# Optimization experiments

Hardware: AMD Instinct MI355X
Metric: run time of the kernel (lower is better)

## Reference

```python
import jax, jax.numpy as jnp
import numpy as np

D_MODEL = 768
NUM_HEADS = 12
D_K = D_MODEL // NUM_HEADS
WINDOW = 16
SPARSITY = 0.8
NEG = -1e9


def _pos_encoding(seq_len, d_model, dtype):
    pos = jnp.arange(seq_len, dtype=jnp.float32)[:, None]
    div = jnp.exp(jnp.arange(0, d_model, 2, dtype=jnp.float32) * (-np.log(10000.0) / d_model))
    pe = jnp.zeros((seq_len, d_model), dtype=jnp.float32)
    pe = pe.at[:, 0::2].set(jnp.sin(pos * div))
    pe = pe.at[:, 1::2].set(jnp.cos(pos * div))
    return pe.astype(dtype)


def _layernorm(x, gamma, beta, eps=1e-5):
    mu = jnp.mean(x, axis=-1, keepdims=True)
    var = jnp.mean(jnp.square(x - mu), axis=-1, keepdims=True)
    return (x - mu) * jax.lax.rsqrt(var + eps) * gamma + beta


def _split_heads(x):  # [B,S,D] -> [B,H,S,dk]
    b, s, _ = x.shape
    return x.reshape(b, s, NUM_HEADS, D_K).transpose(0, 2, 1, 3)


def _attn(q, k, v, mask):  # mask broadcastable to [B,H,S,S], bool
    scores = jnp.einsum('bhqd,bhkd->bhqk', q, k) / jnp.sqrt(jnp.asarray(D_K, q.dtype))
    scores = jnp.where(mask, scores, jnp.asarray(NEG, q.dtype))
    w = jax.nn.softmax(scores, axis=-1)
    out = jnp.einsum('bhqk,bhkd->bhqd', w, v)
    b, h, s, d = out.shape
    return out.transpose(0, 2, 1, 3).reshape(b, s, h * d)


def setup_inputs() -> dict:
    key = jax.random.key(0)
    ks = jax.random.split(key, 16)
    d = D_MODEL
    sc = 1.0 / np.sqrt(d)
    inp = {
        'x': jax.random.normal(ks[0], (2, 2048, d), jnp.float32),
        'wgq': jax.random.normal(ks[1], (d, d), jnp.float32) * sc,
        'wgk': jax.random.normal(ks[2], (d, d), jnp.float32) * sc,
        'wgv': jax.random.normal(ks[3], (d, d), jnp.float32) * sc,
        'wlq': jax.random.normal(ks[4], (d, d), jnp.float32) * sc,
        'wlk': jax.random.normal(ks[5], (d, d), jnp.float32) * sc,
        'wlv': jax.random.normal(ks[6], (d, d), jnp.float32) * sc,
        'wtq': jax.random.normal(ks[7], (d, d), jnp.float32) * sc,
        'wtk': jax.random.normal(ks[8], (d, d), jnp.float32) * sc,
        'wtv': jax.random.normal(ks[9], (d, d), jnp.float32) * sc,
        'w_out': jax.random.normal(ks[10], (3 * d, d), jnp.float32) * (1.0 / np.sqrt(3 * d)),
        'b_out': jnp.zeros((d,), jnp.float32),
        'w_gate': jax.random.normal(ks[11], (d, 3), jnp.float32) * sc,
        'b_gate': jnp.zeros((3,), jnp.float32),
        'w_sparse': jax.random.normal(ks[12], (d, 1), jnp.float32) * sc,
        'b_sparse': jnp.zeros((1,), jnp.float32),
        'g_gamma': jnp.ones((d,), jnp.float32), 'g_beta': jnp.zeros((d,), jnp.float32),
        'l_gamma': jnp.ones((d,), jnp.float32), 'l_beta': jnp.zeros((d,), jnp.float32),
        't_gamma': jnp.ones((d,), jnp.float32), 't_beta': jnp.zeros((d,), jnp.float32),
    }
    return inp


def reference(x, wgq, wgk, wgv, wlq, wlk, wlv, wtq, wtk, wtv,
              w_out, b_out, w_gate, b_gate, w_sparse, b_sparse,
              g_gamma, g_beta, l_gamma, l_beta, t_gamma, t_beta):
    b, s, d = x.shape
    # positional encoding branch input (dropout is identity at eval)
    x_pos = x + _pos_encoding(s, d, x.dtype)[None]

    # focus gate over mean-pooled tokens -> [B,3]
    fw = jax.nn.softmax(x.mean(axis=1) @ w_gate + b_gate, axis=-1)
    gw, lw, tw = fw[:, 0, None, None], fw[:, 1, None, None], fw[:, 2, None, None]

    # sparse (global) mask: keep top-k important columns per batch
    importance = (x @ w_sparse + b_sparse)[..., 0]  # [B,S]
    k = max(1, int((1.0 - SPARSITY) * s))
    _, topk_idx = jax.lax.top_k(importance, k)
    sparse = jnp.zeros((b, s), bool).at[jnp.arange(b)[:, None], topk_idx].set(True)
    sparse_mask = sparse[:, None, None, :]  # [B,1,1,S]

    idx = jnp.arange(s)
    rel = idx[None, :] - idx[:, None]
    half = WINDOW // 2
    local_mask = ((rel >= -half) & (rel <= half))[None, None]  # [1,1,S,S]

    stride = max(1, s // 8)
    temporal_cols = (idx % stride) == 0
    temporal_mask = jnp.broadcast_to(temporal_cols[None, :], (s, s))[None, None]

    # global branch
    g = _attn(_split_heads(x @ wgq), _split_heads(x @ wgk), _split_heads(x @ wgv), sparse_mask)
    g = _layernorm(g, g_gamma, g_beta)
    # local branch
    l = _attn(_split_heads(x @ wlq), _split_heads(x @ wlk), _split_heads(x @ wlv), local_mask)
    l = _layernorm(l, l_gamma, l_beta)
    # temporal branch (uses pos-encoded input)
    t = _attn(_split_heads(x_pos @ wtq), _split_heads(x_pos @ wtk), _split_heads(x_pos @ wtv), temporal_mask)
    t = _layernorm(t, t_gamma, t_beta)

    combined = jnp.concatenate([g * gw, l * lw, t * tw], axis=-1)
    return combined @ w_out + b_out
```

## Files before the change

### kernel.cpp

```cpp
#include <hip/hip_runtime.h>
#include <cstdint>

constexpr int BB   = 2;
constexpr int SS   = 2048;
constexpr int DD   = 768;
constexpr int HH   = 12;
constexpr int NTOK = BB * SS;
constexpr int KSEL = 409;
constexpr int KPAD = 448;
constexpr int NKT  = 7;

typedef __bf16 bf16x8 __attribute__((ext_vector_type(8)));
typedef float  f32x4  __attribute__((ext_vector_type(4)));

__device__ __forceinline__ float b2f(unsigned short u) {
  return __uint_as_float(((unsigned)u) << 16);
}
__device__ __forceinline__ unsigned short f2b(float f) {
  unsigned u = __float_as_uint(f);
  u += 0x7fffu + ((u >> 16) & 1u);
  return (unsigned short)(u >> 16);
}
__device__ __forceinline__ unsigned long long shfl_xor_u64(unsigned long long v, int m) {
  unsigned lo = (unsigned)v, hi = (unsigned)(v >> 32);
  lo = __shfl_xor(lo, m, 64);
  hi = __shfl_xor(hi, m, 64);
  return ((unsigned long long)hi << 32) | lo;
}

__device__ __forceinline__ void gload_lds16(const void* gsrc, void* ldst) {
  __builtin_amdgcn_global_load_lds(
      (__attribute__((address_space(1))) void*)(gsrc),
      (__attribute__((address_space(3))) void*)(ldst), 16, 0, 0);
}

__global__ __launch_bounds__(256) void prep_imp(const float* __restrict__ x,
                                                const float* __restrict__ wsp,
                                                const float* __restrict__ bsp,
                                                unsigned short* __restrict__ xb,
                                                unsigned short* __restrict__ xpb,
                                                float* __restrict__ imp) {
  int srow = blockIdx.x;
  int tid = threadIdx.x;
  const float* xr0 = x + (long)srow * DD;
  const float* xr1 = x + (long)(SS + srow) * DD;
  float acc0 = 0.f, acc1 = 0.f;
#pragma unroll
  for (int k = 0; k < 3; ++k) {
    int c = tid + k * 256;
    int j2 = c & ~1;
    float freq = __expf((float)j2 * -0.011992630692677323f);
    float ang = (float)srow * freq;
    float pe = (c & 1) ? cosf(ang) : sinf(ang);
    float w = wsp[c];
    float x0 = xr0[c], x1 = xr1[c];
    xb[(long)srow * DD + c]        = f2b(x0);
    xb[(long)(SS + srow) * DD + c] = f2b(x1);
    xpb[(long)srow * DD + c]        = f2b(x0 + pe);
    xpb[(long)(SS + srow) * DD + c] = f2b(x1 + pe);
    acc0 += x0 * w;
    acc1 += x1 * w;
  }
#pragma unroll
  for (int m = 1; m < 64; m <<= 1) {
    acc0 += __shfl_xor(acc0, m, 64);
    acc1 += __shfl_xor(acc1, m, 64);
  }
  __shared__ float red[8];
  int wv = tid >> 6, lane = tid & 63;
  if (lane == 0) { red[wv] = acc0; red[4 + wv] = acc1; }
  __syncthreads();
  if (tid == 0) {
    imp[srow]      = red[0] + red[1] + red[2] + red[3] + bsp[0];
    imp[SS + srow] = red[4] + red[5] + red[6] + red[7] + bsp[0];
  }
}

__global__ void transpose_all(const float* w0, const float* w1, const float* w2,
                              const float* w3, const float* w4, const float* w5,
                              const float* w6, const float* w7, const float* w8,
                              const float* w9,
                              unsigned short* WTx4, unsigned short* WTkv,
                              unsigned short* WTqt, unsigned short* WTtkv,
                              unsigned short* WTo) {
  __shared__ float tile[32][33];
  int id = blockIdx.x;
  int z, bx, by;
  if (id < 5184) { z = id / 576; int rem = id % 576; by = rem / 24; bx = rem % 24; }
  else           { z = 9; int rem = id - 5184; by = rem / 24; bx = rem % 24; }
  const float* srcs[10] = {w0, w1, w2, w3, w4, w5, w6, w7, w8, w9};
  const float* src = srcs[z];
  unsigned short* dst;
  int R = DD;
  switch (z) {
    case 0: dst = WTx4;                       break;
    case 1: dst = WTkv;                       break;
    case 2: dst = WTkv + (long)DD * DD;       break;
    case 3: dst = WTx4 + (long)DD * DD;       break;
    case 4: dst = WTx4 + (long)2 * DD * DD;   break;
    case 5: dst = WTx4 + (long)3 * DD * DD;   break;
    case 6: dst = WTqt;                       break;
    case 7: dst = WTtkv;                      break;
    case 8: dst = WTtkv + (long)DD * DD;      break;
    default: dst = WTo; R = 2304;             break;
  }
  int r0 = by * 32;
  int c0 = bx * 32;
  int tx = threadIdx.x, ty = threadIdx.y;
  for (int i = ty; i < 32; i += 8) tile[i][tx] = src[(long)(r0 + i) * DD + c0 + tx];
  __syncthreads();
  for (int i = ty; i < 32; i += 8) dst[(long)(c0 + i) * R + r0 + tx] = f2b(tile[tx][i]);
}

__global__ __launch_bounds__(1024) void topk_kernel(const float* __restrict__ imp,
                                                    int* __restrict__ sel) {
  __shared__ unsigned long long keys[SS];
  int b = blockIdx.x, tid = threadIdx.x;
  for (int i = tid; i < SS; i += 1024) {
    float v = imp[b * SS + i];
    unsigned u = __float_as_uint(v);
    u = (u & 0x80000000u) ? ~u : (u | 0x80000000u);
    unsigned du = ~u;
    keys[i] = ((unsigned long long)du << 32) | (unsigned)i;
  }
  __syncthreads();
  for (int k = 2; k <= SS; k <<= 1) {
    for (int j = k >> 1; j >= 64; j >>= 1) {
      for (int i = tid; i < SS; i += 1024) {
        int p = i ^ j;
        if (p > i) {
          unsigned long long a = keys[i], bb = keys[p];
          bool up = ((i & k) == 0);
          if ((a > bb) == up) { keys[i] = bb; keys[p] = a; }
        }
      }
      __syncthreads();
    }
    unsigned long long k0 = keys[tid], k1 = keys[tid + 1024];
    bool up0 = ((tid & k) == 0);
    bool up1 = (((tid + 1024) & k) == 0);
    int j0 = (k >> 1) < 32 ? (k >> 1) : 32;
    for (int j = j0; j >= 1; j >>= 1) {
      bool low = ((tid & j) == 0);
      unsigned long long p0 = shfl_xor_u64(k0, j);
      k0 = ((low == up0) == (k0 < p0)) ? k0 : p0;
      unsigned long long p1 = shfl_xor_u64(k1, j);
      k1 = ((low == up1) == (k1 < p1)) ? k1 : p1;
    }
    keys[tid] = k0; keys[tid + 1024] = k1;
    __syncthreads();
  }
  for (int i = tid; i < KSEL; i += 1024) sel[b * KSEL + i] = (int)(keys[i] & 0xffffffffu);
}

__global__ __launch_bounds__(256) void gate1(const float* __restrict__ x,
                                             float* __restrict__ partial) {
  int b = blockIdx.y, chunk = blockIdx.x, tid = threadIdx.x;
  for (int c = tid; c < DD; c += 256) {
    const float* xp = x + ((long)(b * SS + chunk * 128)) * DD + c;
    float acc = 0.f;
    for (int s2 = 0; s2 < 128; ++s2) acc += xp[(long)s2 * DD];
    partial[(long)(b * 16 + chunk) * DD + c] = acc;
  }
}

__global__ __launch_bounds__(256) void gate2(const float* __restrict__ partial,
                                             const float* __restrict__ w_gate,
                                             const float* __restrict__ b_gate,
                                             float* __restrict__ fw) {
  int b = blockIdx.x, tid = threadIdx.x;
  __shared__ float meanbuf[DD];
  __shared__ float lg[3];
  for (int c = tid; c < DD; c += 256) {
    float acc = 0.f;
    for (int p = 0; p < 16; ++p) acc += partial[(long)(b * 16 + p) * DD + c];
    meanbuf[c] = acc * (1.0f / (float)SS);
  }
  __syncthreads();
  if (tid < 3) {
    float acc = b_gate[tid];
    for (int d = 0; d < DD; ++d) acc += meanbuf[d] * w_gate[d * 3 + tid];
    lg[tid] = acc;
  }
  __syncthreads();
  if (tid == 0) {
    float mx = fmaxf(lg[0], fmaxf(lg[1], lg[2]));
    float e0 = expf(lg[0] - mx), e1 = expf(lg[1] - mx), e2 = expf(lg[2] - mx);
    float inv = 1.f / (e0 + e1 + e2);
    fw[b * 3 + 0] = e0 * inv; fw[b * 3 + 1] = e1 * inv; fw[b * 3 + 2] = e2 * inv;
  }
}

__global__ __launch_bounds__(192) void gather_pre(const unsigned short* __restrict__ xb,
                                                  const unsigned short* __restrict__ xpb,
                                                  const int* __restrict__ sel,
                                                  unsigned short* __restrict__ A_sel,
                                                  unsigned short* __restrict__ A_t8) {
  int id = blockIdx.x;
  int tid = threadIdx.x;
  if (id < BB * KPAD) {
    int b = id / KPAD, j = id % KPAD;
    uint2* dst = (uint2*)(A_sel + (long)id * DD);
    if (j < KSEL) {
      const uint2* src = (const uint2*)(xb + (long)(b * SS + sel[b * KSEL + j]) * DD);
      dst[tid] = src[tid];
    } else {
      dst[tid] = uint2{0u, 0u};
    }
  } else {
    int r = id - BB * KPAD;
    uint2* dst = (uint2*)(A_t8 + (long)r * DD);
    if (r < 16) {
      int b = r >> 3, j = (r & 7) * 256;
      const uint2* src = (const uint2*)(xpb + (long)(b * SS + j) * DD);
      dst[tid] = src[tid];
    } else {
      dst[tid] = uint2{0u, 0u};
    }
  }
}

__global__ __launch_bounds__(256) void gemm_multi(
    const unsigned short* __restrict__ xb,    const unsigned short* __restrict__ WTx4,
    unsigned short* __restrict__ QKV4,
    const unsigned short* __restrict__ A_sel, const unsigned short* __restrict__ WTkv,
    unsigned short* __restrict__ KVg,
    const unsigned short* __restrict__ xpb,   const unsigned short* __restrict__ WTqt,
    unsigned short* __restrict__ Qt,
    const unsigned short* __restrict__ A_t8,  const unsigned short* __restrict__ WTtkv,
    unsigned short* __restrict__ K8, unsigned short* __restrict__ Vt8,
    unsigned short* __restrict__ Vt, unsigned short* __restrict__ Vtl) {
  __shared__ unsigned short smem[16512];
  unsigned short* AsB = smem;
  unsigned short* BsB = smem + 8192;
  constexpr int K = DD;
  const int tid = threadIdx.x;
  const int lane = tid & 63;
  const int wv = tid >> 6;
  const int wr = wv >> 1, wc = wv & 1;

  int lin = blockIdx.x;
  int swz = (lin & 7) * 132 + (lin >> 3);
  const unsigned short *A, *BT;
  unsigned short* C;
  int N, ntx, tile, mode;
  if (swz < 768)       { A = xb;    BT = WTx4;  C = QKV4; N = 3072; ntx = 24; tile = swz;
                         mode = ((tile % 24) >= 18) ? 1 : 0; }
  else if (swz < 852)  { A = A_sel; BT = WTkv;  C = KVg;  N = 1536; ntx = 12; tile = swz - 768;
                         mode = ((tile % 12) >= 6) ? 2 : 0; }
  else if (swz < 1044) { A = xpb;   BT = WTqt;  C = Qt;   N = 768;  ntx = 6;  tile = swz - 852;
                         mode = 0; }
  else                 { A = A_t8;  BT = WTtkv; C = nullptr; N = 1536; ntx = 12; tile = swz - 1044;
                         mode = ((tile % 12) >= 6) ? 4 : 3; }
  const long rowBase = (long)(tile / ntx) * 128;
  const long colBase = (long)(tile % ntx) * 128;
  const int vcol0 = (mode == 1) ? (int)colBase - 2304
                  : (mode == 2 || mode == 4) ? (int)colBase - 768 : 0;

  f32x4 acc[4][4];
#pragma unroll
  for (int i = 0; i < 4; ++i)
#pragma unroll
    for (int j = 0; j < 4; ++j)
#pragma unroll
      for (int r = 0; r < 4; ++r) acc[i][j][r] = 0.f;

  const int g0 = tid, g1 = tid + 256;
  const int r0 = g0 >> 2, k80 = (g0 & 3) ^ ((r0 >> 1) & 3);
  const int r1 = g1 >> 2, k81 = (g1 & 3) ^ ((r1 >> 1) & 3);
  const unsigned short* ga0 = A + (rowBase + r0) * (long)K + k80 * 8;
  const unsigned short* ga1 = A + (rowBase + r1) * (long)K + k81 * 8;
  const unsigned short* gb0 = BT + (colBase + r0) * (long)K + k80 * 8;
  const unsigned short* gb1 = BT + (colBase + r1) * (long)K + k81 * 8;

  const int k8 = lane >> 4;
  const int fr = lane & 15;
  int aoff[4], boff[4];
#pragma unroll
  for (int i = 0; i < 4; ++i) {
    int rowA = wr * 64 + i * 16 + fr;
    aoff[i] = (rowA * 4 + (k8 ^ ((rowA >> 1) & 3))) * 8;
    int rowB = wc * 64 + i * 16 + fr;
    boff[i] = (rowB * 4 + (k8 ^ ((rowB >> 1) & 3))) * 8;
  }

  auto stage = [&](int buf, int t) {
    int ko = t * 32;
    gload_lds16(ga0 + ko, &AsB[buf * 4096 + g0 * 8]);
    gload_lds16(ga1 + ko, &AsB[buf * 4096 + g1 * 8]);
    gload_lds16(gb0 + ko, &BsB[buf * 4096 + g0 * 8]);
    gload_lds16(gb1 + ko, &BsB[buf * 4096 + g1 * 8]);
  };

  constexpr int nk = K >> 5;
  stage(0, 0);
  __syncthreads();
  for (int t = 0; t < nk; ++t) {
    int cur = t & 1;
    if (t + 1 < nk) stage(cur ^ 1, t + 1);
    bf16x8 af[4], bfr[4];
#pragma unroll
    for (int i = 0; i < 4; ++i) af[i] = *(const bf16x8*)(&AsB[cur * 4096 + aoff[i]]);
#pragma unroll
    for (int i = 0; i < 4; ++i) bfr[i] = *(const bf16x8*)(&BsB[cur * 4096 + boff[i]]);
#pragma unroll
    for (int mi = 0; mi < 4; ++mi)
#pragma unroll
      for (int ni = 0; ni < 4; ++ni)
        acc[mi][ni] = __builtin_amdgcn_mfma_f32_16x16x32_bf16(af[mi], bfr[ni], acc[mi][ni], 0, 0, 0);
    __syncthreads();
  }

  const int orow0 = (lane >> 4) * 4;
  if (mode == 0) {
#pragma unroll
    for (int mi = 0; mi < 4; ++mi) {
      long gr = rowBase + wr * 64 + mi * 16 + orow0;
#pragma unroll
      for (int ni = 0; ni < 4; ++ni) {
        long gc = colBase + wc * 64 + ni * 16 + fr;
#pragma unroll
        for (int r = 0; r < 4; ++r)
          C[(gr + r) * (long)N + gc] = f2b(acc[mi][ni][r]);
      }
    }
  } else {
    unsigned short* Ct = smem;
#pragma unroll
    for (int mi = 0; mi < 4; ++mi) {
      int lr = wr * 64 + mi * 16 + orow0;
#pragma unroll
      for (int ni = 0; ni < 4; ++ni) {
        int lc = wc * 64 + ni * 16 + fr;
#pragma unroll
        for (int r = 0; r < 4; ++r)
          Ct[(lr + r) * 129 + lc] = f2b(acc[mi][ni][r]);
      }
    }
    __syncthreads();
    if (mode == 1) {
#pragma unroll
      for (int e = 0; e < 8; ++e) {
        int id = tid + e * 256;
        int c = id >> 4, sc = id & 15;
        int grow = (int)rowBase + sc * 8;
        int bb2 = grow >> 11, s = grow & (SS - 1);
        union { unsigned short s8[8]; uint4 v; } u;
#pragma unroll
        for (int k2 = 0; k2 < 8; ++k2) u.s8[k2] = Ct[(sc * 8 + k2) * 129 + c];
        *(uint4*)(Vtl + ((long)bb2 * DD + vcol0 + c) * SS + s) = u.v;
      }
    } else if (mode == 2) {
#pragma unroll
      for (int e = 0; e < 8; ++e) {
        int id = tid + e * 256;
        int c = id >> 4, sc = id & 15;
        int grow = (int)rowBase + sc * 8;
        int bb2 = grow / KPAD, j = grow % KPAD;
        union { unsigned short s8[8]; uint4 v; } u;
#pragma unroll
        for (int k2 = 0; k2 < 8; ++k2) u.s8[k2] = Ct[(sc * 8 + k2) * 129 + c];
        *(uint4*)(Vt + ((long)bb2 * DD + vcol0 + c) * KPAD + j) = u.v;
      }
    } else if (mode == 3) {
#pragma unroll
      for (int e = 0; e < 2; ++e) {
        int id = tid + e * 256;
        int row = id >> 4;
        int bb2 = row >> 4, jj = row & 15;
        int c8 = id & 15;
        int srcrow = (jj < 8) ? bb2 * 8 + jj : 16 + jj;
        union { unsigned short s8[8]; uint4 v; } u;
#pragma unroll
        for (int k2 = 0; k2 < 8; ++k2) u.s8[k2] = Ct[srcrow * 129 + c8 * 8 + k2];
        *(uint4*)(K8 + ((long)bb2 * 16 + jj) * DD + colBase + c8 * 8) = u.v;
      }
    } else {
#pragma unroll
      for (int e = 0; e < 4; ++e) {
        int id = tid + e * 256;
        int bb2 = id >> 9;
        int rem = id & 511;
        int c = rem >> 2, jc = rem & 3;
        union { unsigned short s8[8]; uint4 v; } u;
        if (jc == 0) {
#pragma unroll
          for (int k2 = 0; k2 < 8; ++k2) u.s8[k2] = Ct[(bb2 * 8 + k2) * 129 + c];
        } else {
#pragma unroll
          for (int k2 = 0; k2 < 8; ++k2) u.s8[k2] = 0;
        }
        *(uint4*)(Vt8 + ((long)bb2 * DD + vcol0 + c) * 32 + jc * 8) = u.v;
      }
    }
  }
}

__global__ __launch_bounds__(256) void gemm_final_sk(const unsigned short* __restrict__ A,
                                                     const unsigned short* __restrict__ BT,
                                                     float* __restrict__ Cpart) {
  __shared__ unsigned short As[2][128 * 32];
  __shared__ unsigned short Bs[2][128 * 32];
  constexpr int N = 768, K = 2304, CK = 768;
  const int tid = threadIdx.x;
  const int lane = tid & 63;
  const int wv = tid >> 6;
  const int wr = wv >> 1, wc = wv & 1;
  const int z = blockIdx.z;

  int lin = blockIdx.y * gridDim.x + blockIdx.x;
  int swz = (lin & 7) * 24 + (lin >> 3);
  const long rowBase = (long)(swz / 6) * 128;
  const long colBase = (long)(swz % 6) * 128;

  f32x4 acc[4][4];
#pragma unroll
  for (int i = 0; i < 4; ++i)
#pragma unroll
    for (int j = 0; j < 4; ++j)
#pragma unroll
      for (int r = 0; r < 4; ++r) acc[i][j][r] = 0.f;

  const int g0 = tid, g1 = tid + 256;
  const int r0 = g0 >> 2, k80 = (g0 & 3) ^ ((r0 >> 1) & 3);
  const int r1 = g1 >> 2, k81 = (g1 & 3) ^ ((r1 >> 1) & 3);
  const unsigned short* ga0 = A + (rowBase + r0) * (long)K + z * CK + k80 * 8;
  const unsigned short* ga1 = A + (rowBase + r1) * (long)K + z * CK + k81 * 8;
  const unsigned short* gb0 = BT + (colBase + r0) * (long)K + z * CK + k80 * 8;
  const unsigned short* gb1 = BT + (colBase + r1) * (long)K + z * CK + k81 * 8;

  const int k8 = lane >> 4;
  const int fr = lane & 15;
  int aoff[4], boff[4];
#pragma unroll
  for (int i = 0; i < 4; ++i) {
    int rowA = wr * 64 + i * 16 + fr;
    aoff[i] = (rowA * 4 + (k8 ^ ((rowA >> 1) & 3))) * 8;
    int rowB = wc * 64 + i * 16 + fr;
    boff[i] = (rowB * 4 + (k8 ^ ((rowB >> 1) & 3))) * 8;
  }

  auto stage = [&](int buf, int t) {
    int ko = t * 32;
    gload_lds16(ga0 + ko, &As[buf][g0 * 8]);
    gload_lds16(ga1 + ko, &As[buf][g1 * 8]);
    gload_lds16(gb0 + ko, &Bs[buf][g0 * 8]);
    gload_lds16(gb1 + ko, &Bs[buf][g1 * 8]);
  };

  constexpr int nk = CK >> 5;
  stage(0, 0);
  __syncthreads();
  for (int t = 0; t < nk; ++t) {
    int cur = t & 1;
    if (t + 1 < nk) stage(cur ^ 1, t + 1);
    bf16x8 af[4], bfr[4];
#pragma unroll
    for (int i = 0; i < 4; ++i) af[i] = *(const bf16x8*)(&As[cur][aoff[i]]);
#pragma unroll
    for (int i = 0; i < 4; ++i) bfr[i] = *(const bf16x8*)(&Bs[cur][boff[i]]);
#pragma unroll
    for (int mi = 0; mi < 4; ++mi)
#pragma unroll
      for (int ni = 0; ni < 4; ++ni)
        acc[mi][ni] = __builtin_amdgcn_mfma_f32_16x16x32_bf16(af[mi], bfr[ni], acc[mi][ni], 0, 0, 0);
    __syncthreads();
  }

  float* Cz = Cpart + (long)z * NTOK * DD;
  const int orow0 = (lane >> 4) * 4;
#pragma unroll
  for (int mi = 0; mi < 4; ++mi) {
    long gr = rowBase + wr * 64 + mi * 16 + orow0;
#pragma unroll
    for (int ni = 0; ni < 4; ++ni) {
      long gc = colBase + wc * 64 + ni * 16 + fr;
#pragma unroll
      for (int r = 0; r < 4; ++r)
        Cz[(gr + r) * (long)N + gc] = acc[mi][ni][r];
    }
  }
}

__global__ __launch_bounds__(256) void reduce_out(const float* __restrict__ P,
                                                  const float* __restrict__ bias,
                                                  float* __restrict__ out) {
  long i = (long)blockIdx.x * 256 + threadIdx.x;
  const f32x4* p0 = (const f32x4*)P;
  const f32x4* p1 = (const f32x4*)(P + (long)NTOK * DD);
  const f32x4* p2 = (const f32x4*)(P + 2L * NTOK * DD);
  f32x4 v = p0[i];
  v += p1[i];
  v += p2[i];
  int c4 = (int)(i % (DD / 4));
  v += *(const f32x4*)(bias + c4 * 4);
  ((f32x4*)out)[i] = v;
}

__device__ __forceinline__ void attn_flash_body(
    const unsigned short* __restrict__ QKV4,
    const unsigned short* __restrict__ KVg,
    const unsigned short* __restrict__ Vt,
    float* __restrict__ Outp,
    unsigned short* smem) {
  unsigned short* Kl = smem;
  unsigned short* Vl = smem + 8192;
  unsigned short* Pl = smem + 16384;
  int tid = threadIdx.x, w = tid >> 6, lane = tid & 63;
  int fr = lane & 15, g = lane >> 4;
  int b = blockIdx.y / HH, h = blockIdx.y % HH, hoff = h * 64;
  int qbase = blockIdx.x * 64 + w * 16;
  long qrow = (long)b * SS + qbase + fr;

  const unsigned short* qptr = QKV4 + qrow * 3072 + hoff + g * 8;
  bf16x8 bq0 = *(const bf16x8*)(qptr);
  bf16x8 bq1 = *(const bf16x8*)(qptr + 32);

  const int s0 = tid, s1 = tid + 256;
  const int r0 = s0 >> 3, c0 = (s0 & 7) ^ (r0 & 7);
  const int r1 = s1 >> 3, c1 = (s1 & 7) ^ (r1 & 7);
  const unsigned short* kg_b = KVg + (long)b * KPAD * 1536 + hoff;
  const unsigned short* vt_b = Vt + ((long)b * DD + hoff) * KPAD;

  auto stage = [&](int buf, int t0) {
    gload_lds16(kg_b + (long)(t0 * 64 + r0) * 1536 + c0 * 8, &Kl[buf * 4096 + s0 * 8]);
    gload_lds16(kg_b + (long)(t0 * 64 + r1) * 1536 + c1 * 8, &Kl[buf * 4096 + s1 * 8]);
    gload_lds16(vt_b + (long)r0 * KPAD + t0 * 64 + c0 * 8, &Vl[buf * 4096 + s0 * 8]);
    gload_lds16(vt_b + (long)r1 * KPAD + t0 * 64 + c1 * 8, &Vl[buf * 4096 + s1 * 8]);
  };

  f32x4 oacc[4];
#pragma unroll
  for (int mf = 0; mf < 4; ++mf)
#pragma unroll
    for (int r = 0; r < 4; ++r) oacc[mf][r] = 0.f;
  float m = -3.0e38f, l = 0.f;

  stage(0, 0);
  asm volatile("s_waitcnt vmcnt(0)" ::: "memory");
  __syncthreads();

  for (int t = 0; t < NKT; ++t) {
    int cur = t & 1;
    if (t + 1 < NKT) stage(cur ^ 1, t + 1);

    f32x4 st[4];
#pragma unroll
    for (int kt = 0; kt < 4; ++kt) {
      int row = kt * 16 + fr;
      bf16x8 a0 = *(const bf16x8*)(&Kl[cur * 4096 + (row * 8 + (g ^ (row & 7))) * 8]);
      bf16x8 a1 = *(const bf16x8*)(&Kl[cur * 4096 + (row * 8 + ((4 + g) ^ (row & 7))) * 8]);
      f32x4 z = {0.f, 0.f, 0.f, 0.f};
      z = __builtin_amdgcn_mfma_f32_16x16x32_bf16(a0, bq0, z, 0, 0, 0);
      st[kt] = __builtin_amdgcn_mfma_f32_16x16x32_bf16(a1, bq1, z, 0, 0, 0);
    }

    float tm = -3.0e38f;
#pragma unroll
    for (int kt = 0; kt < 4; ++kt)
#pragma unroll
      for (int r = 0; r < 4; ++r) {
        int key = t * 64 + kt * 16 + g * 4 + r;
        float s = (key < KSEL) ? st[kt][r] * 0.125f : -1.0e30f;
        st[kt][r] = s;
        tm = fmaxf(tm, s);
      }
    tm = fmaxf(tm, __shfl_xor(tm, 16, 64));
    tm = fmaxf(tm, __shfl_xor(tm, 32, 64));
    float newm = fmaxf(m, tm);
    float f = __expf(m - newm);
    float tsum = 0.f;
#pragma unroll
    for (int kt = 0; kt < 4; ++kt)
#pragma unroll
      for (int r = 0; r < 4; ++r) {
        float e = __expf(st[kt][r] - newm);
        st[kt][r] = e;
        tsum += e;
      }
    tsum += __shfl_xor(tsum, 16, 64);
    tsum += __shfl_xor(tsum, 32, 64);
    l = l * f + tsum;
    m = newm;
#pragma unroll
    for (int mf = 0; mf < 4; ++mf)
#pragma unroll
      for (int r = 0; r < 4; ++r) oacc[mf][r] *= f;

    unsigned short* pw = &Pl[w * 1088 + fr * 68 + g * 4];
#pragma unroll
    for (int kt = 0; kt < 4; ++kt) {
      uint2 pk;
      pk.x = (unsigned)f2b(st[kt][0]) | ((unsigned)f2b(st[kt][1]) << 16);
      pk.y = (unsigned)f2b(st[kt][2]) | ((unsigned)f2b(st[kt][3]) << 16);
      *(uint2*)(pw + kt * 16) = pk;
    }

    const unsigned short* prd = &Pl[w * 1088 + fr * 68];
#pragma unroll
    for (int ks2 = 0; ks2 < 2; ++ks2) {
      bf16x8 pf = *(const bf16x8*)(prd + ks2 * 32 + g * 8);
#pragma unroll
      for (int mf = 0; mf < 4; ++mf) {
        int vr = mf * 16 + fr;
        int vc = ks2 * 4 + g;
        bf16x8 vf = *(const bf16x8*)(&Vl[cur * 4096 + (vr * 8 + (vc ^ (vr & 7))) * 8]);
        oacc[mf] = __builtin_amdgcn_mfma_f32_16x16x32_bf16(vf, pf, oacc[mf], 0, 0, 0);
      }
    }

    asm volatile("s_waitcnt vmcnt(0)" ::: "memory");
    __syncthreads();
  }

  float inv = 1.f / l;
  float* orow = Outp + qrow * DD + hoff;
#pragma unroll
  for (int mf = 0; mf < 4; ++mf) {
    f32x4 ov;
#pragma unroll
    for (int r = 0; r < 4; ++r) ov[r] = oacc[mf][r] * inv;
    *(f32x4*)(orow + mf * 16 + g * 4) = ov;
  }
}

__device__ __forceinline__ void attn_win_body(
    const unsigned short* __restrict__ QKV,
    const unsigned short* __restrict__ K8,
    const unsigned short* __restrict__ Vt,
    float* __restrict__ Outp,
    int LD, int QO, long VSTR, bool local,
    unsigned short* smem) {
  int tid = threadIdx.x, w = tid >> 6, lane = tid & 63;
  int fr = lane & 15, g = lane >> 4;
  int b = blockIdx.y / HH, h = blockIdx.y % HH, hoff = h * 64;
  int qbase = blockIdx.x * 64 + w * 16;
  long qrow = (long)b * SS + qbase + fr;

  const unsigned short* qptr = QKV + qrow * LD + QO + hoff + g * 8;
  bf16x8 bq0 = *(const bf16x8*)(qptr);
  bf16x8 bq1 = *(const bf16x8*)(qptr + 32);

  int kstart = qbase - 8;
  if (kstart < 0) kstart = 0;
  if (kstart > SS - 32) kstart = SS - 32;

  f32x4 st[2];
  if (local) {
#pragma unroll
    for (int kt = 0; kt < 2; ++kt) {
      const unsigned short* kp =
          QKV + ((long)b * SS + kstart + kt * 16 + fr) * LD + 1536 + hoff + g * 8;
      bf16x8 a0 = *(const bf16x8*)(kp);
      bf16x8 a1 = *(const bf16x8*)(kp + 32);
      f32x4 z = {0.f, 0.f, 0.f, 0.f};
      z = __builtin_amdgcn_mfma_f32_16x16x32_bf16(a0, bq0, z, 0, 0, 0);
      st[kt] = __builtin_amdgcn_mfma_f32_16x16x32_bf16(a1, bq1, z, 0, 0, 0);
    }
  } else {
    const unsigned short* kp = K8 + ((long)b * 16 + fr) * DD + hoff + g * 8;
    bf16x8 a0 = *(const bf16x8*)(kp);
    bf16x8 a1 = *(const bf16x8*)(kp + 32);
    f32x4 z = {0.f, 0.f, 0.f, 0.f};
    z = __builtin_amdgcn_mfma_f32_16x16x32_bf16(a0, bq0, z, 0, 0, 0);
    st[0] = __builtin_amdgcn_mfma_f32_16x16x32_bf16(a1, bq1, z, 0, 0, 0);
    st[1] = f32x4{0.f, 0.f, 0.f, 0.f};
  }

  float m = -3.0e38f;
#pragma unroll
  for (int kt = 0; kt < 2; ++kt)
#pragma unroll
    for (int r = 0; r < 4; ++r) {
      int idx = kt * 16 + g * 4 + r;
      bool valid;
      if (local) {
        int rel = kstart + idx - qbase - fr;
        valid = (rel >= -8) && (rel <= 8);
      } else {
        valid = (idx < 8);
      }
      float s = valid ? st[kt][r] * 0.125f : -1.0e30f;
      st[kt][r] = s;
      m = fmaxf(m, s);
    }
  m = fmaxf(m, __shfl_xor(m, 16, 64));
  m = fmaxf(m, __shfl_xor(m, 32, 64));

  float lsum = 0.f;
#pragma unroll
  for (int kt = 0; kt < 2; ++kt)
#pragma unroll
    for (int r = 0; r < 4; ++r) {
      float e = __expf(st[kt][r] - m);
      st[kt][r] = e;
      lsum += e;
    }
  lsum += __shfl_xor(lsum, 16, 64);
  lsum += __shfl_xor(lsum, 32, 64);

  unsigned short* pl = smem + w * 640 + fr * 40 + g * 4;
#pragma unroll
  for (int kt = 0; kt < 2; ++kt) {
    uint2 pk;
    pk.x = (unsigned)f2b(st[kt][0]) | ((unsigned)f2b(st[kt][1]) << 16);
    pk.y = (unsigned)f2b(st[kt][2]) | ((unsigned)f2b(st[kt][3]) << 16);
    *(uint2*)(pl + kt * 16) = pk;
  }

  f32x4 oacc[4];
#pragma unroll
  for (int mf = 0; mf < 4; ++mf)
#pragma unroll
    for (int r = 0; r < 4; ++r) oacc[mf][r] = 0.f;

  const unsigned short* pr = smem + w * 640 + fr * 40 + g * 8;
  bf16x8 pf = *(const bf16x8*)(pr);
  long kb2 = local ? kstart : 0;
#pragma unroll
  for (int mf = 0; mf < 4; ++mf) {
    const unsigned short* vp =
        Vt + ((long)b * DD + hoff + mf * 16 + fr) * VSTR + kb2 + g * 8;
    bf16x8 vf = *(const bf16x8*)(vp);
    oacc[mf] = __builtin_amdgcn_mfma_f32_16x16x32_bf16(vf, pf, oacc[mf], 0, 0, 0);
  }

  float inv = 1.f / lsum;
  float* orow = Outp + qrow * DD + hoff;
#pragma unroll
  for (int mf = 0; mf < 4; ++mf) {
    f32x4 ov;
#pragma unroll
    for (int r = 0; r < 4; ++r) ov[r] = oacc[mf][r] * inv;
    *(f32x4*)(orow + mf * 16 + g * 4) = ov;
  }
}

__global__ __launch_bounds__(256) void attn_all(
    const unsigned short* __restrict__ QKV4,
    const unsigned short* __restrict__ KVg,
    const unsigned short* __restrict__ Vt,
    const unsigned short* __restrict__ Qt,
    const unsigned short* __restrict__ K8,
    const unsigned short* __restrict__ Vt8,
    const unsigned short* __restrict__ Vtl,
    float* __restrict__ gout, float* __restrict__ lout, float* __restrict__ tout) {
  __shared__ unsigned short smem[20736];
  int z = blockIdx.z;
  if (z == 0) {
    attn_flash_body(QKV4, KVg, Vt, gout, smem);
  } else if (z == 1) {
    attn_win_body(QKV4, nullptr, Vtl, lout, 3072, 768, SS, true, smem);
  } else {
    attn_win_body(Qt, K8, Vt8, tout, 768, 0, 32, false, smem);
  }
}

__global__ __launch_bounds__(256) void ln_gate_concat(
    const float* __restrict__ gsrc, const float* __restrict__ lsrc, const float* __restrict__ tsrc,
    const float* __restrict__ gg, const float* __restrict__ gb,
    const float* __restrict__ lgam, const float* __restrict__ lbet,
    const float* __restrict__ tg, const float* __restrict__ tb,
    const float* __restrict__ fw, unsigned short* __restrict__ comb) {
  int row = blockIdx.x;
  int b = row >> 11;
  int tid = threadIdx.x;
  __shared__ float red[8];
  const float* srcs[3] = {gsrc, lsrc, tsrc};
  const float* gams[3] = {gg, lgam, tg};
  const float* bets[3] = {gb, lbet, tb};
#pragma unroll
  for (int br = 0; br < 3; ++br) {
    const float* src = srcs[br] + (long)row * DD;
    float x0 = src[tid], x1 = src[tid + 256], x2 = src[tid + 512];
    float s = x0 + x1 + x2;
    float ss = x0 * x0 + x1 * x1 + x2 * x2;
#pragma unroll
    for (int msk = 1; msk < 64; msk <<= 1) {
      s += __shfl_xor(s, msk, 64);
      ss += __shfl_xor(ss, msk, 64);
    }
    int wv = tid >> 6, lane = tid & 63;
    if (lane == 0) { red[wv] = s; red[4 + wv] = ss; }
    __syncthreads();
    float S4 = red[0] + red[1] + red[2] + red[3];
    float SQ = red[4] + red[5] + red[6] + red[7];
    float mean = S4 * (1.f / (float)DD);
    float var = SQ * (1.f / (float)DD) - mean * mean;
    float rs = rsqrtf(var + 1e-5f);
    float gate = fw[b * 3 + br];
    const float* gam = gams[br];
    const float* bet = bets[br];
    unsigned short* dst = comb + (long)row * 2304 + br * DD;
    dst[tid]       = f2b(((x0 - mean) * rs * gam[tid]       + bet[tid])       * gate);
    dst[tid + 256] = f2b(((x1 - mean) * rs * gam[tid + 256] + bet[tid + 256]) * gate);
    dst[tid + 512] = f2b(((x2 - mean) * rs * gam[tid + 512] + bet[tid + 512]) * gate);
    __syncthreads();
  }
}

extern "C" void kernel_launch(void* const* d_in, const int* in_sizes, int n_in,
                              void* d_out, int out_size, void* d_ws, size_t ws_size,
                              hipStream_t stream) {
  const float* x        = (const float*)d_in[0];
  const float* wgq      = (const float*)d_in[1];
  const float* wgk      = (const float*)d_in[2];
  const float* wgv      = (const float*)d_in[3];
  const float* wlq      = (const float*)d_in[4];
  const float* wlk      = (const float*)d_in[5];
  const float* wlv      = (const float*)d_in[6];
  const float* wtq      = (const float*)d_in[7];
  const float* wtk      = (const float*)d_in[8];
  const float* wtv      = (const float*)d_in[9];
  const float* w_out    = (const float*)d_in[10];
  const float* b_out    = (const float*)d_in[11];
  const float* w_gate   = (const float*)d_in[12];
  const float* b_gate   = (const float*)d_in[13];
  const float* w_sparse = (const float*)d_in[14];
  const float* b_sparse = (const float*)d_in[15];
  const float* g_gamma  = (const float*)d_in[16];
  const float* g_beta   = (const float*)d_in[17];
  const float* l_gamma  = (const float*)d_in[18];
  const float* l_beta   = (const float*)d_in[19];
  const float* t_gamma  = (const float*)d_in[20];
  const float* t_beta   = (const float*)d_in[21];
  float* outp = (float*)d_out;

  unsigned short* xb    = (unsigned short*)d_ws;
  unsigned short* xpb   = xb    + (long)NTOK * DD;
  unsigned short* WTx4  = xpb   + (long)NTOK * DD;
  unsigned short* WTkv  = WTx4  + (long)3072 * DD;
  unsigned short* WTqt  = WTkv  + (long)1536 * DD;
  unsigned short* WTtkv = WTqt  + (long)DD * DD;
  unsigned short* WTo   = WTtkv + (long)1536 * DD;
  unsigned short* QKV4  = WTo   + (long)DD * 2304;
  unsigned short* Qt    = QKV4  + (long)NTOK * 3072;
  unsigned short* A_sel = Qt    + (long)NTOK * DD;
  unsigned short* KVg   = A_sel + (long)BB * KPAD * DD;
  unsigned short* A_t8  = KVg   + (long)BB * KPAD * 1536;
  unsigned short* K8    = A_t8  + (long)128 * DD;
  unsigned short* Vt8   = K8    + (long)BB * 16 * DD;
  unsigned short* Vt    = Vt8   + (long)BB * DD * 32;
  unsigned short* Vtl   = Vt    + (long)BB * DD * KPAD;
  unsigned short* comb  = Vtl   + (long)BB * DD * SS;
  float* gout    = (float*)(comb + (long)NTOK * 2304);
  float* lout    = gout + (long)NTOK * DD;
  float* tout    = lout + (long)NTOK * DD;
  float* imp     = tout + (long)NTOK * DD;
  float* partial = imp + NTOK;
  float* fw      = partial + 32 * DD;
  int*   sel     = (int*)(fw + 8);
  float* Cpart = gout;

  prep_imp<<<SS, 256, 0, stream>>>(x, w_sparse, b_sparse, xb, xpb, imp);
  transpose_all<<<6912, dim3(32, 8), 0, stream>>>(
      wgq, wgk, wgv, wlq, wlk, wlv, wtq, wtk, wtv, w_out,
      WTx4, WTkv, WTqt, WTtkv, WTo);
  topk_kernel<<<BB, 1024, 0, stream>>>(imp, sel);
  gate1<<<dim3(16, BB), 256, 0, stream>>>(x, partial);
  gate2<<<BB, 256, 0, stream>>>(partial, w_gate, b_gate, fw);

  gather_pre<<<BB * KPAD + 128, 192, 0, stream>>>(xb, xpb, sel, A_sel, A_t8);
  gemm_multi<<<1056, 256, 0, stream>>>(xb, WTx4, QKV4, A_sel, WTkv, KVg,
                                       xpb, WTqt, Qt, A_t8, WTtkv,
                                       K8, Vt8, Vt, Vtl);

  attn_all<<<dim3(32, BB * HH, 3), 256, 0, stream>>>(QKV4, KVg, Vt, Qt, K8, Vt8,
                                                     Vtl, gout, lout, tout);

  ln_gate_concat<<<NTOK, 256, 0, stream>>>(gout, lout, tout, g_gamma, g_beta,
                                           l_gamma, l_beta, t_gamma, t_beta, fw, comb);
  gemm_final_sk<<<dim3(6, 32, 3), 256, 0, stream>>>(comb, WTo, Cpart);
  reduce_out<<<NTOK * DD / 4 / 256, 256, 0, stream>>>(Cpart, b_out, outp);
}
```

Baseline: 205.5 us.

## Write attention outputs as bf16 into concat buffer, drop LDS transpose epilogue

Attention kernels now write bf16 outputs straight into the combined concat buffer, and layernorm+gate runs in place on it. This removes the fp32 gout/lout/tout intermediates and their extra global traffic. The QKV GEMM epilogue drops the LDS-staged transpose and scatters packed 4-element stores directly to the transposed V layouts. gate1 also reads the bf16 copy of x instead of fp32. The costs are extra bf16 rounding before layernorm, and direct transposed stores that may coalesce worse than the staged ones.

```diff
diff --git a/kernel.cpp b/kernel.cpp
--- a/kernel.cpp
+++ b/kernel.cpp
@@ -153,13 +153,13 @@
   for (int i = tid; i < KSEL; i += 1024) sel[b * KSEL + i] = (int)(keys[i] & 0xffffffffu);
 }
 
-__global__ __launch_bounds__(256) void gate1(const float* __restrict__ x,
+__global__ __launch_bounds__(256) void gate1(const unsigned short* __restrict__ xb,
                                              float* __restrict__ partial) {
   int b = blockIdx.y, chunk = blockIdx.x, tid = threadIdx.x;
   for (int c = tid; c < DD; c += 256) {
-    const float* xp = x + ((long)(b * SS + chunk * 128)) * DD + c;
+    const unsigned short* xp = xb + ((long)(b * SS + chunk * 128)) * DD + c;
     float acc = 0.f;
-    for (int s2 = 0; s2 < 128; ++s2) acc += xp[(long)s2 * DD];
+    for (int s2 = 0; s2 < 128; ++s2) acc += b2f(xp[(long)s2 * DD]);
     partial[(long)(b * 16 + chunk) * DD + c] = acc;
   }
 }
@@ -230,9 +230,8 @@
     const unsigned short* __restrict__ A_t8,  const unsigned short* __restrict__ WTtkv,
     unsigned short* __restrict__ K8, unsigned short* __restrict__ Vt8,
     unsigned short* __restrict__ Vt, unsigned short* __restrict__ Vtl) {
-  __shared__ unsigned short smem[16512];
-  unsigned short* AsB = smem;
-  unsigned short* BsB = smem + 8192;
+  __shared__ unsigned short AsB[2][4096];
+  __shared__ unsigned short BsB[2][4096];
   constexpr int K = DD;
   const int tid = threadIdx.x;
   const int lane = tid & 63;
@@ -242,20 +241,13 @@
   int lin = blockIdx.x;
   int swz = (lin & 7) * 132 + (lin >> 3);
   const unsigned short *A, *BT;
-  unsigned short* C;
-  int N, ntx, tile, mode;
-  if (swz < 768)       { A = xb;    BT = WTx4;  C = QKV4; N = 3072; ntx = 24; tile = swz;
-                         mode = ((tile % 24) >= 18) ? 1 : 0; }
-  else if (swz < 852)  { A = A_sel; BT = WTkv;  C = KVg;  N = 1536; ntx = 12; tile = swz - 768;
-                         mode = ((tile % 12) >= 6) ? 2 : 0; }
-  else if (swz < 1044) { A = xpb;   BT = WTqt;  C = Qt;   N = 768;  ntx = 6;  tile = swz - 852;
-                         mode = 0; }
-  else                 { A = A_t8;  BT = WTtkv; C = nullptr; N = 1536; ntx = 12; tile = swz - 1044;
-                         mode = ((tile % 12) >= 6) ? 4 : 3; }
+  int ntx, tile;
+  if (swz < 768)       { A = xb;    BT = WTx4;  ntx = 24; tile = swz; }
+  else if (swz < 852)  { A = A_sel; BT = WTkv;  ntx = 12; tile = swz - 768; }
+  else if (swz < 1044) { A = xpb;   BT = WTqt;  ntx = 6;  tile = swz - 852; }
+  else                 { A = A_t8;  BT = WTtkv; ntx = 12; tile = swz - 1044; }
   const long rowBase = (long)(tile / ntx) * 128;
   const long colBase = (long)(tile % ntx) * 128;
-  const int vcol0 = (mode == 1) ? (int)colBase - 2304
-                  : (mode == 2 || mode == 4) ? (int)colBase - 768 : 0;
 
   f32x4 acc[4][4];
 #pragma unroll
@@ -286,10 +278,10 @@
 
   auto stage = [&](int buf, int t) {
     int ko = t * 32;
-    gload_lds16(ga0 + ko, &AsB[buf * 4096 + g0 * 8]);
-    gload_lds16(ga1 + ko, &AsB[buf * 4096 + g1 * 8]);
-    gload_lds16(gb0 + ko, &BsB[buf * 4096 + g0 * 8]);
-    gload_lds16(gb1 + ko, &BsB[buf * 4096 + g1 * 8]);
+    gload_lds16(ga0 + ko, &AsB[buf][g0 * 8]);
+    gload_lds16(ga1 + ko, &AsB[buf][g1 * 8]);
+    gload_lds16(gb0 + ko, &BsB[buf][g0 * 8]);
+    gload_lds16(gb1 + ko, &BsB[buf][g1 * 8]);
   };
 
   constexpr int nk = K >> 5;
@@ -300,9 +292,9 @@
     if (t + 1 < nk) stage(cur ^ 1, t + 1);
     bf16x8 af[4], bfr[4];
 #pragma unroll
-    for (int i = 0; i < 4; ++i) af[i] = *(const bf16x8*)(&AsB[cur * 4096 + aoff[i]]);
-#pragma unroll
-    for (int i = 0; i < 4; ++i) bfr[i] = *(const bf16x8*)(&BsB[cur * 4096 + boff[i]]);
+    for (int i = 0; i < 4; ++i) af[i] = *(const bf16x8*)(&AsB[cur][aoff[i]]);
+#pragma unroll
+    for (int i = 0; i < 4; ++i) bfr[i] = *(const bf16x8*)(&BsB[cur][boff[i]]);
 #pragma unroll
     for (int mi = 0; mi < 4; ++mi)
 #pragma unroll
@@ -311,6 +303,16 @@
     __syncthreads();
   }
 
+  int mode, vcol0 = 0, N = 0;
+  unsigned short* C = nullptr;
+  if (swz < 768)       { mode = (colBase >= 2304) ? 1 : 0; C = QKV4; N = 3072;
+                         vcol0 = (int)colBase - 2304; }
+  else if (swz < 852)  { mode = (colBase >= 768) ? 2 : 0;  C = KVg;  N = 1536;
+                         vcol0 = (int)colBase - 768; }
+  else if (swz < 1044) { mode = 0; C = Qt; N = 768; }
+  else                 { mode = (colBase >= 768) ? 4 : 3;
+                         vcol0 = (int)colBase - 768; }
+
   const int orow0 = (lane >> 4) * 4;
   if (mode == 0) {
 #pragma unroll
@@ -325,72 +327,51 @@
       }
     }
   } else {
-    unsigned short* Ct = smem;
 #pragma unroll
     for (int mi = 0; mi < 4; ++mi) {
       int lr = wr * 64 + mi * 16 + orow0;
+      int grow = (int)rowBase + lr;
 #pragma unroll
       for (int ni = 0; ni < 4; ++ni) {
         int lc = wc * 64 + ni * 16 + fr;
-#pragma unroll
-        for (int r = 0; r < 4; ++r)
-          Ct[(lr + r) * 129 + lc] = f2b(acc[mi][ni][r]);
+        uint2 pk;
+        pk.x = (unsigned)f2b(acc[mi][ni][0]) | ((unsigned)f2b(acc[mi][ni][1]) << 16);
+        pk.y = (unsigned)f2b(acc[mi][ni][2]) | ((unsigned)f2b(acc[mi][ni][3]) << 16);
+        if (mode == 1) {
+          int bb2 = grow >> 11, s = grow & (SS - 1);
+          *(uint2*)(Vtl + ((long)bb2 * DD + vcol0 + lc) * SS + s) = pk;
+        } else if (mode == 2) {
+          int bb2 = grow / KPAD, j = grow - bb2 * KPAD;
+          *(uint2*)(Vt + ((long)bb2 * DD + vcol0 + lc) * KPAD + j) = pk;
+        } else if (mode == 3) {
+          if (grow < 16) {
+#pragma unroll
+            for (int r = 0; r < 4; ++r) {
+              int g2 = grow + r;
+              K8[((long)(g2 >> 3) * 16 + (g2 & 7)) * DD + colBase + lc] =
+                  f2b(acc[mi][ni][r]);
+            }
+          }
+        } else {
+          if (grow < 16) {
+            *(uint2*)(Vt8 + ((long)(grow >> 3) * DD + vcol0 + lc) * 32 + (grow & 7)) = pk;
+          }
+        }
       }
     }
-    __syncthreads();
-    if (mode == 1) {
-#pragma unroll
-      for (int e = 0; e < 8; ++e) {
+    if (mode == 3) {
+      int row16 = tid >> 4, cg = tid & 15;
+      int bb2 = row16 >> 3, jj = 8 + (row16 & 7);
+      uint4 z4 = {0u, 0u, 0u, 0u};
+      *(uint4*)(K8 + ((long)bb2 * 16 + jj) * DD + colBase + cg * 8) = z4;
+    }
+    if (mode == 4) {
+#pragma unroll
+      for (int e = 0; e < 6; ++e) {
         int id = tid + e * 256;
-        int c = id >> 4, sc = id & 15;
-        int grow = (int)rowBase + sc * 8;
-        int bb2 = grow >> 11, s = grow & (SS - 1);
-        union { unsigned short s8[8]; uint4 v; } u;
-#pragma unroll
-        for (int k2 = 0; k2 < 8; ++k2) u.s8[k2] = Ct[(sc * 8 + k2) * 129 + c];
-        *(uint4*)(Vtl + ((long)bb2 * DD + vcol0 + c) * SS + s) = u.v;
-      }
-    } else if (mode == 2) {
-#pragma unroll
-      for (int e = 0; e < 8; ++e) {
-        int id = tid + e * 256;
-        int c = id >> 4, sc = id & 15;
-        int grow = (int)rowBase + sc * 8;
-        int bb2 = grow / KPAD, j = grow % KPAD;
-        union { unsigned short s8[8]; uint4 v; } u;
-#pragma unroll
-        for (int k2 = 0; k2 < 8; ++k2) u.s8[k2] = Ct[(sc * 8 + k2) * 129 + c];
-        *(uint4*)(Vt + ((long)bb2 * DD + vcol0 + c) * KPAD + j) = u.v;
-      }
-    } else if (mode == 3) {
-#pragma unroll
-      for (int e = 0; e < 2; ++e) {
-        int id = tid + e * 256;
-        int row = id >> 4;
-        int bb2 = row >> 4, jj = row & 15;
-        int c8 = id & 15;
-        int srcrow = (jj < 8) ? bb2 * 8 + jj : 16 + jj;
-        union { unsigned short s8[8]; uint4 v; } u;
-#pragma unroll
-        for (int k2 = 0; k2 < 8; ++k2) u.s8[k2] = Ct[srcrow * 129 + c8 * 8 + k2];
-        *(uint4*)(K8 + ((long)bb2 * 16 + jj) * DD + colBase + c8 * 8) = u.v;
-      }
-    } else {
-#pragma unroll
-      for (int e = 0; e < 4; ++e) {
-        int id = tid + e * 256;
-        int bb2 = id >> 9;
-        int rem = id & 511;
-        int c = rem >> 2, jc = rem & 3;
-        union { unsigned short s8[8]; uint4 v; } u;
-        if (jc == 0) {
-#pragma unroll
-          for (int k2 = 0; k2 < 8; ++k2) u.s8[k2] = Ct[(bb2 * 8 + k2) * 129 + c];
-        } else {
-#pragma unroll
-          for (int k2 = 0; k2 < 8; ++k2) u.s8[k2] = 0;
-        }
-        *(uint4*)(Vt8 + ((long)bb2 * DD + vcol0 + c) * 32 + jc * 8) = u.v;
+        int bb2 = id / 768, rem = id % 768;
+        int c = rem / 6, ch = rem % 6;
+        *(uint2*)(Vt8 + ((long)bb2 * DD + vcol0 + c) * 32 + 8 + ch * 4) = uint2{0u, 0u};
       }
     }
   }
@@ -501,7 +482,7 @@
     const unsigned short* __restrict__ QKV4,
     const unsigned short* __restrict__ KVg,
     const unsigned short* __restrict__ Vt,
-    float* __restrict__ Outp,
+    unsigned short* __restrict__ comb,
     unsigned short* smem) {
   unsigned short* Kl = smem;
   unsigned short* Vl = smem + 8192;
@@ -614,13 +595,13 @@
   }
 
   float inv = 1.f / l;
-  float* orow = Outp + qrow * DD + hoff;
+  unsigned short* orow = comb + qrow * 2304 + hoff;
 #pragma unroll
   for (int mf = 0; mf < 4; ++mf) {
-    f32x4 ov;
-#pragma unroll
-    for (int r = 0; r < 4; ++r) ov[r] = oacc[mf][r] * inv;
-    *(f32x4*)(orow + mf * 16 + g * 4) = ov;
+    uint2 pk;
+    pk.x = (unsigned)f2b(oacc[mf][0] * inv) | ((unsigned)f2b(oacc[mf][1] * inv) << 16);
+    pk.y = (unsigned)f2b(oacc[mf][2] * inv) | ((unsigned)f2b(oacc[mf][3] * inv) << 16);
+    *(uint2*)(orow + mf * 16 + g * 4) = pk;
   }
 }
 
@@ -628,7 +609,7 @@
     const unsigned short* __restrict__ QKV,
     const unsigned short* __restrict__ K8,
     const unsigned short* __restrict__ Vt,
-    float* __restrict__ Outp,
+    unsigned short* __restrict__ comb, int brOff,
     int LD, int QO, long VSTR, bool local,
     unsigned short* smem) {
   int tid = threadIdx.x, w = tid >> 6, lane = tid & 63;
@@ -726,13 +707,13 @@
   }
 
   float inv = 1.f / lsum;
-  float* orow = Outp + qrow * DD + hoff;
+  unsigned short* orow = comb + qrow * 2304 + brOff + hoff;
 #pragma unroll
   for (int mf = 0; mf < 4; ++mf) {
-    f32x4 ov;
-#pragma unroll
-    for (int r = 0; r < 4; ++r) ov[r] = oacc[mf][r] * inv;
-    *(f32x4*)(orow + mf * 16 + g * 4) = ov;
+    uint2 pk;
+    pk.x = (unsigned)f2b(oacc[mf][0] * inv) | ((unsigned)f2b(oacc[mf][1] * inv) << 16);
+    pk.y = (unsigned)f2b(oacc[mf][2] * inv) | ((unsigned)f2b(oacc[mf][3] * inv) << 16);
+    *(uint2*)(orow + mf * 16 + g * 4) = pk;
   }
 }
 
@@ -744,35 +725,34 @@
     const unsigned short* __restrict__ K8,
     const unsigned short* __restrict__ Vt8,
     const unsigned short* __restrict__ Vtl,
-    float* __restrict__ gout, float* __restrict__ lout, float* __restrict__ tout) {
+    unsigned short* __restrict__ comb) {
   __shared__ unsigned short smem[20736];
   int z = blockIdx.z;
   if (z == 0) {
-    attn_flash_body(QKV4, KVg, Vt, gout, smem);
+    attn_flash_body(QKV4, KVg, Vt, comb, smem);
   } else if (z == 1) {
-    attn_win_body(QKV4, nullptr, Vtl, lout, 3072, 768, SS, true, smem);
+    attn_win_body(QKV4, nullptr, Vtl, comb, 768, 3072, 768, SS, true, smem);
   } else {
-    attn_win_body(Qt, K8, Vt8, tout, 768, 0, 32, false, smem);
-  }
-}
-
-__global__ __launch_bounds__(256) void ln_gate_concat(
-    const float* __restrict__ gsrc, const float* __restrict__ lsrc, const float* __restrict__ tsrc,
+    attn_win_body(Qt, K8, Vt8, comb, 1536, 768, 0, 32, false, smem);
+  }
+}
+
+__global__ __launch_bounds__(256) void ln_gate_inplace(
+    unsigned short* __restrict__ comb,
     const float* __restrict__ gg, const float* __restrict__ gb,
     const float* __restrict__ lgam, const float* __restrict__ lbet,
     const float* __restrict__ tg, const float* __restrict__ tb,
-    const float* __restrict__ fw, unsigned short* __restrict__ comb) {
+    const float* __restrict__ fw) {
   int row = blockIdx.x;
   int b = row >> 11;
   int tid = threadIdx.x;
   __shared__ float red[8];
-  const float* srcs[3] = {gsrc, lsrc, tsrc};
   const float* gams[3] = {gg, lgam, tg};
   const float* bets[3] = {gb, lbet, tb};
 #pragma unroll
   for (int br = 0; br < 3; ++br) {
-    const float* src = srcs[br] + (long)row * DD;
-    float x0 = src[tid], x1 = src[tid + 256], x2 = src[tid + 512];
+    unsigned short* p = comb + (long)row * 2304 + br * DD;
+    float x0 = b2f(p[tid]), x1 = b2f(p[tid + 256]), x2 = b2f(p[tid + 512]);
     float s = x0 + x1 + x2;
     float ss = x0 * x0 + x1 * x1 + x2 * x2;
 #pragma unroll
@@ -791,10 +771,9 @@
     float gate = fw[b * 3 + br];
     const float* gam = gams[br];
     const float* bet = bets[br];
-    unsigned short* dst = comb + (long)row * 2304 + br * DD;
-    dst[tid]       = f2b(((x0 - mean) * rs * gam[tid]       + bet[tid])       * gate);
-    dst[tid + 256] = f2b(((x1 - mean) * rs * gam[tid + 256] + bet[tid + 256]) * gate);
-    dst[tid + 512] = f2b(((x2 - mean) * rs * gam[tid + 512] + bet[tid + 512]) * gate);
+    p[tid]       = f2b(((x0 - mean) * rs * gam[tid]       + bet[tid])       * gate);
+    p[tid + 256] = f2b(((x1 - mean) * rs * gam[tid + 256] + bet[tid + 256]) * gate);
+    p[tid + 512] = f2b(((x2 - mean) * rs * gam[tid + 512] + bet[tid + 512]) * gate);
     __syncthreads();
   }
 }
@@ -843,21 +822,18 @@
   unsigned short* Vt    = Vt8   + (long)BB * DD * 32;
   unsigned short* Vtl   = Vt    + (long)BB * DD * KPAD;
   unsigned short* comb  = Vtl   + (long)BB * DD * SS;
-  float* gout    = (float*)(comb + (long)NTOK * 2304);
-  float* lout    = gout + (long)NTOK * DD;
-  float* tout    = lout + (long)NTOK * DD;
-  float* imp     = tout + (long)NTOK * DD;
+  float* Cpart   = (float*)(comb + (long)NTOK * 2304);
+  float* imp     = Cpart + 3L * NTOK * DD;
   float* partial = imp + NTOK;
   float* fw      = partial + 32 * DD;
   int*   sel     = (int*)(fw + 8);
-  float* Cpart = gout;
 
   prep_imp<<<SS, 256, 0, stream>>>(x, w_sparse, b_sparse, xb, xpb, imp);
   transpose_all<<<6912, dim3(32, 8), 0, stream>>>(
       wgq, wgk, wgv, wlq, wlk, wlv, wtq, wtk, wtv, w_out,
       WTx4, WTkv, WTqt, WTtkv, WTo);
   topk_kernel<<<BB, 1024, 0, stream>>>(imp, sel);
-  gate1<<<dim3(16, BB), 256, 0, stream>>>(x, partial);
+  gate1<<<dim3(16, BB), 256, 0, stream>>>(xb, partial);
   gate2<<<BB, 256, 0, stream>>>(partial, w_gate, b_gate, fw);
 
   gather_pre<<<BB * KPAD + 128, 192, 0, stream>>>(xb, xpb, sel, A_sel, A_t8);
@@ -866,10 +842,10 @@
                                        K8, Vt8, Vt, Vtl);
 
   attn_all<<<dim3(32, BB * HH, 3), 256, 0, stream>>>(QKV4, KVg, Vt, Qt, K8, Vt8,
-                                                     Vtl, gout, lout, tout);
-
-  ln_gate_concat<<<NTOK, 256, 0, stream>>>(gout, lout, tout, g_gamma, g_beta,
-                                           l_gamma, l_beta, t_gamma, t_beta, fw, comb);
+                                                     Vtl, comb);
+
+  ln_gate_inplace<<<NTOK, 256, 0, stream>>>(comb, g_gamma, g_beta,
+                                            l_gamma, l_beta, t_gamma, t_beta, fw);
   gemm_final_sk<<<dim3(6, 32, 3), 256, 0, stream>>>(comb, WTo, Cpart);
   reduce_out<<<NTOK * DD / 4 / 256, 256, 0, stream>>>(Cpart, b_out, outp);
 }
```

After: 203.5 us. Within noise of the previous version (-1.0%).
